# Kernel optimization log

Hardware: AMD Instinct MI355X
Metric: run time of the kernel (lower is better)

The kernel has to match this reference:

```python
import jax, jax.numpy as jnp
import numpy as np

# dims
N, E, H, ED, G = 50000, 1000000, 64, 16, 512
IN_C, OUT_C, L, T, OUT_N = 39, 128, 3, 2, 1
SLOPE = 0.01  # negative slope used by F.leaky_relu and GATConv(negative_slope=0.01)


def _seg_softmax(a, seg, n):
    # numerically-stable softmax over edges grouped by target segment
    m = jax.ops.segment_max(a, seg, num_segments=n)
    m = jnp.where(jnp.isfinite(m), m, 0.0)
    e = jnp.exp(a - m[seg])
    s = jax.ops.segment_sum(e, seg, num_segments=n)
    return e / (s[seg] + 1e-16)


def _gru(inp, h, wi, wh, bi, bh):
    # torch.nn.GRUCell: gates ordered (r, z, n)
    gi = inp @ wi.T + bi
    gh = h @ wh.T + bh
    ir, iz, i_n = jnp.split(gi, 3, axis=-1)
    hr, hz, h_n = jnp.split(gh, 3, axis=-1)
    r = jax.nn.sigmoid(ir + hr)
    z = jax.nn.sigmoid(iz + hz)
    n = jnp.tanh(i_n + r * h_n)
    return (1.0 - z) * n + z * h


def _forward(x, edge_attr,
             lin1_w, lin1_b,
             g_lin1_w, g_att_l, g_att_r, g_lin2_w, g_bias,
             gru0_wi, gru0_wh, gru0_bi, gru0_bh,
             conv_lin_w, conv_att_src, conv_att_dst, conv_bias,
             grul_wi, grul_wh, grul_bi, grul_bh,
             mol_lin_w, mol_att_src, mol_att_dst, mol_bias,
             mgru_wi, mgru_wh, mgru_bi, mgru_bh,
             lin2_w, lin2_b,
             src, dst, batch):
    x = jax.nn.leaky_relu(x @ lin1_w.T + lin1_b, SLOPE)  # [N,H]

    # ---- GATEConv ----
    xj, xi = x[src], x[dst]                               # [E,H]
    t = jax.nn.leaky_relu(jnp.concatenate([xj, edge_attr], -1) @ g_lin1_w.T, SLOPE)
    a = jax.nn.leaky_relu(t @ g_att_l + xi @ g_att_r, SLOPE)
    a = _seg_softmax(a, dst, N)
    h = jax.ops.segment_sum((xj @ g_lin2_w.T) * a[:, None], dst, num_segments=N) + g_bias
    h = jax.nn.elu(h)
    x = jax.nn.relu(_gru(h, x, gru0_wi, gru0_wh, gru0_bi, gru0_bh))

    # ---- GATConv atom layers ----
    for l in range(L - 1):
        hs = x @ conv_lin_w[l].T                          # [N,H]
        a = jax.nn.leaky_relu((hs @ conv_att_src[l])[src] + (hs @ conv_att_dst[l])[dst], SLOPE)
        a = _seg_softmax(a, dst, N)
        h = jax.ops.segment_sum(hs[src] * a[:, None], dst, num_segments=N) + conv_bias[l]
        h = jax.nn.elu(h)
        x = jax.nn.relu(_gru(h, x, grul_wi[l], grul_wh[l], grul_bi[l], grul_bh[l]))

    # ---- molecule-level attention readout ----
    out = jax.nn.relu(jax.ops.segment_sum(x, batch, num_segments=G))  # [G,H]
    for _ in range(T):
        hs = x @ mol_lin_w.T                              # [N,H]  (atoms = sources)
        hd = out @ mol_lin_w.T                            # [G,H]  (mols = targets)
        a = jax.nn.leaky_relu(hs @ mol_att_src + (hd @ mol_att_dst)[batch], SLOPE)
        a = _seg_softmax(a, batch, G)
        h = jax.ops.segment_sum(hs * a[:, None], batch, num_segments=G) + mol_bias
        h = jax.nn.elu(h)
        out = jax.nn.relu(_gru(h, out, mgru_wi, mgru_wh, mgru_bi, mgru_bh))

    out = out @ lin2_w.T + lin2_b                         # [G,OUT_C]
    return jnp.concatenate([out[None]] * OUT_N, axis=0)   # [OUT_N,G,OUT_C]


def setup_inputs() -> dict:
    key = jax.random.key(0)
    it = iter(jax.random.split(key, 48))

    def p(*shape):
        return jax.random.normal(next(it), shape, jnp.float32) * 0.1

    d = {}
    d["x"] = jax.random.normal(next(it), (N, IN_C), jnp.float32)
    d["edge_index"] = jax.random.randint(next(it), (2, E), 0, N, dtype=jnp.int32)
    d["edge_attr"] = jax.random.normal(next(it), (E, ED), jnp.float32)
    d["batch"] = jnp.sort(jax.random.randint(next(it), (N,), 0, G, dtype=jnp.int32))

    d["lin1_w"], d["lin1_b"] = p(H, IN_C), p(H)
    d["g_lin1_w"] = p(H, H + ED)
    d["g_att_l"], d["g_att_r"] = p(H), p(H)
    d["g_lin2_w"], d["g_bias"] = p(H, H), p(H)
    d["gru0_wi"], d["gru0_wh"] = p(3 * H, H), p(3 * H, H)
    d["gru0_bi"], d["gru0_bh"] = p(3 * H), p(3 * H)
    d["conv_lin_w"] = p(L - 1, H, H)
    d["conv_att_src"], d["conv_att_dst"] = p(L - 1, H), p(L - 1, H)
    d["conv_bias"] = p(L - 1, H)
    d["grul_wi"], d["grul_wh"] = p(L - 1, 3 * H, H), p(L - 1, 3 * H, H)
    d["grul_bi"], d["grul_bh"] = p(L - 1, 3 * H), p(L - 1, 3 * H)
    d["mol_lin_w"] = p(H, H)
    d["mol_att_src"], d["mol_att_dst"] = p(H), p(H)
    d["mol_bias"] = p(H)
    d["mgru_wi"], d["mgru_wh"] = p(3 * H, H), p(3 * H, H)
    d["mgru_bi"], d["mgru_bh"] = p(3 * H), p(3 * H)
    d["lin2_w"], d["lin2_b"] = p(OUT_C, H), p(OUT_C)
    return d


def reference(x, edge_index, edge_attr, batch,
              lin1_w, lin1_b,
              g_lin1_w, g_att_l, g_att_r, g_lin2_w, g_bias,
              gru0_wi, gru0_wh, gru0_bi, gru0_bh,
              conv_lin_w, conv_att_src, conv_att_dst, conv_bias,
              grul_wi, grul_wh, grul_bi, grul_bh,
              mol_lin_w, mol_att_src, mol_att_dst, mol_bias,
              mgru_wi, mgru_wh, mgru_bi, mgru_bh,
              lin2_w, lin2_b):
    src, dst = edge_index[0], edge_index[1]
    return _forward(x, edge_attr,
                    lin1_w, lin1_b,
                    g_lin1_w, g_att_l, g_att_r, g_lin2_w, g_bias,
                    gru0_wi, gru0_wh, gru0_bi, gru0_bh,
                    conv_lin_w, conv_att_src, conv_att_dst, conv_bias,
                    grul_wi, grul_wh, grul_bi, grul_bh,
                    mol_lin_w, mol_att_src, mol_att_dst, mol_bias,
                    mgru_wi, mgru_wh, mgru_bi, mgru_bh,
                    lin2_w, lin2_b,
                    src, dst, batch)
```

## Files before the change

### kernel.cpp

```cpp
#include <hip/hip_runtime.h>
#include <math.h>

#define N_NODES 50000
#define N_EDGES 1000000
#define NGRAPH  512
#define INC     39
#define NBKT 196
#define BIN_BLK 4096

typedef __attribute__((ext_vector_type(8))) short bf16x8;
typedef __attribute__((ext_vector_type(4))) float f32x4;
typedef __attribute__((ext_vector_type(4))) int i32x4;

__device__ __forceinline__ float lrelu(float x){ return fmaxf(0.01f*x, x); }
__device__ __forceinline__ float fexp(float x){ return __builtin_amdgcn_exp2f(x*1.4426950408889634f); }
__device__ __forceinline__ float frcp(float x){ return __builtin_amdgcn_rcpf(x); }
__device__ __forceinline__ float eluf (float x){ return x > 0.f ? x : fexp(x) - 1.f; }
__device__ __forceinline__ float sigm (float x){ return frcp(1.f + fexp(-x)); }
__device__ __forceinline__ float ftanh(float x){
  x = fminf(fmaxf(x, -15.f), 15.f);
  float e = __builtin_amdgcn_exp2f(x*2.8853900817779268f);
  return (e - 1.f)*frcp(e + 1.f);
}
__device__ __forceinline__ float rdlane(float v, int l){
  return __int_as_float(__builtin_amdgcn_readlane(__float_as_int(v), l));
}
__device__ __forceinline__ unsigned pk_bf16(float a, float b){
  unsigned r;
  asm volatile("v_cvt_pk_bf16_f32 %0, %1, %2" : "=v"(r) : "v"(a), "v"(b));
  return r;
}
__device__ __forceinline__ float bl(unsigned p){ return __uint_as_float(p << 16); }
__device__ __forceinline__ float bh(unsigned p){ return __uint_as_float(p & 0xffff0000u); }
__device__ __forceinline__ float tobf16f(float v){ return __uint_as_float(pk_bf16(v, 0.f) << 16); }

__global__ __launch_bounds__(256) void k_bhist(const int* __restrict__ dst,
                                               int* __restrict__ bcnt) {
  __shared__ int h[NBKT];
  for (int i = threadIdx.x; i < NBKT; i += 256) h[i] = 0;
  __syncthreads();
  const int e0 = blockIdx.x * BIN_BLK;
  #pragma unroll 4
  for (int u = 0; u < 16; ++u) {
    int e = e0 + u*256 + threadIdx.x;
    if (e < N_EDGES) atomicAdd(&h[dst[e] >> 8], 1);
  }
  __syncthreads();
  for (int i = threadIdx.x; i < NBKT; i += 256) if (h[i]) atomicAdd(&bcnt[i], h[i]);
}

__global__ __launch_bounds__(256) void k_bscan(const int* __restrict__ bcnt,
                                               int* __restrict__ bstart,
                                               int* __restrict__ bcur,
                                               int* __restrict__ rowptrN) {
  __shared__ int s[256];
  int t = threadIdx.x;
  int v = (t < NBKT) ? bcnt[t] : 0;
  s[t] = v; __syncthreads();
  for (int off = 1; off < 256; off <<= 1) {
    int x = (t >= off) ? s[t-off] : 0;
    __syncthreads();
    s[t] += x;
    __syncthreads();
  }
  if (t < NBKT) { int st = s[t] - v; bstart[t] = st; bcur[t] = st; }
  if (t == 0) { bstart[NBKT] = N_EDGES; rowptrN[0] = N_EDGES; }
}

__global__ __launch_bounds__(1024) void k_binA(const int* __restrict__ dst,
                                               const int* __restrict__ src,
                                               const float* __restrict__ p,
                                               int* __restrict__ bcur,
                                               int2* __restrict__ binned) {
  __shared__ int lcnt[NBKT];
  __shared__ int lbase[NBKT];
  __shared__ int gbase[NBKT];
  __shared__ int tmp[256];
  __shared__ int totsh;
  __shared__ int2 stage[BIN_BLK];
  const int t = threadIdx.x;
  const int e0 = blockIdx.x * BIN_BLK;
  for (int i = t; i < NBKT; i += 1024) lcnt[i] = 0;
  __syncthreads();
  int myb[4], myr[4], myd[4], mys[4]; float myp[4];
  #pragma unroll
  for (int u = 0; u < 4; ++u) {
    int e = e0 + u*1024 + t;
    if (e < N_EDGES) {
      int d = dst[e];
      myd[u] = d; mys[u] = src[e]; myp[u] = p[e];
      int b = d >> 8;
      myb[u] = b;
      myr[u] = atomicAdd(&lcnt[b], 1);
    } else myb[u] = -1;
  }
  __syncthreads();
  if (t < 256) tmp[t] = (t < NBKT) ? lcnt[t] : 0;
  __syncthreads();
  for (int off = 1; off < 256; off <<= 1) {
    int v = (t >= off && t < 256) ? tmp[t-off] : 0;
    __syncthreads();
    if (t < 256) tmp[t] += v;
    __syncthreads();
  }
  if (t < NBKT) lbase[t] = tmp[t] - lcnt[t];
  if (t == NBKT-1) totsh = tmp[t];
  if (t < NBKT && lcnt[t] > 0) gbase[t] = atomicAdd(&bcur[t], lcnt[t]);
  __syncthreads();
  #pragma unroll
  for (int u = 0; u < 4; ++u) {
    if (myb[u] >= 0) {
      int x = (mys[u] & 0xffff) | ((myd[u] & 255) << 16) | (myb[u] << 24);
      stage[lbase[myb[u]] + myr[u]] = make_int2(x, __float_as_int(myp[u]));
    }
  }
  __syncthreads();
  const int tot = totsh;
  for (int i = t; i < tot; i += 1024) {
    int2 r = stage[i];
    int b = (unsigned)r.x >> 24;
    binned[gbase[b] + (i - lbase[b])] = r;
  }
}

__global__ __launch_bounds__(1024) void k_binB(const int* __restrict__ bstart,
                                               const int2* __restrict__ binned,
                                               int2* __restrict__ sorted,
                                               int* __restrict__ rowptr) {
  __shared__ int lcnt[256];
  __shared__ int loc[256];
  const int b = blockIdx.x;
  const int base = bstart[b], end = bstart[b+1];
  const int t = threadIdx.x;
  if (t < 256) lcnt[t] = 0;
  __syncthreads();
  for (int i = base + t; i < end; i += 1024)
    atomicAdd(&lcnt[(binned[i].x >> 16) & 255], 1);
  __syncthreads();
  if (t < 256) loc[t] = lcnt[t];
  __syncthreads();
  for (int off = 1; off < 256; off <<= 1) {
    int v = (t >= off && t < 256) ? loc[t-off] : 0;
    __syncthreads();
    if (t < 256) loc[t] += v;
    __syncthreads();
  }
  if (t < 256) {
    int st = base + loc[t] - lcnt[t];
    loc[t] = st;
    int node = b*256 + t;
    if (node < N_NODES) rowptr[node] = st;
    lcnt[t] = 0;
  }
  __syncthreads();
  for (int i = base + t; i < end; i += 1024) {
    int2 r = binned[i];
    int dlow = (r.x >> 16) & 255;
    int rank = atomicAdd(&lcnt[dlow], 1);
    sorted[loc[dlow] + rank] = r;
  }
}

__global__ __launch_bounds__(512) void k_gbound(const int* __restrict__ batch,
                                                int* __restrict__ gstart) {
  int g = threadIdx.x;
  int lo = 0, hi = N_NODES;
  while (lo < hi) { int mid = (lo+hi)>>1; if (batch[mid] < g) lo = mid+1; else hi = mid; }
  gstart[g] = lo;
  if (g == 0) gstart[NGRAPH] = N_NODES;
}

__global__ __launch_bounds__(256) void k_wpack(const float* __restrict__ wi,
                                               const float* __restrict__ wh,
                                               unsigned short* __restrict__ o) {
  int i = blockIdx.x*256 + threadIdx.x;
  if (i < 192*64)      o[i]          = (unsigned short)(pk_bf16(wi[i], 0.f) & 0xffffu);
  else if (i < 2*192*64) o[i]        = (unsigned short)(pk_bf16(wh[i - 192*64], 0.f) & 0xffffu);
}

__global__ __launch_bounds__(256) void k_lin1M(const float* __restrict__ x,
                                               const float* __restrict__ W,
                                               const float* __restrict__ b,
                                               const float* __restrict__ v1,
                                               float* __restrict__ out,
                                               float* __restrict__ o1) {
  const int lane = threadIdx.x & 63;
  const int l15 = lane & 15, lg = lane >> 4;
  const int n0 = blockIdx.x*64 + (threadIdx.x >> 6)*16;
  if (n0 >= N_NODES) return;
  union BF { bf16x8 v; unsigned u[4]; };
  BF Bf[3][4];
  #pragma unroll
  for (int c = 0; c < 3; ++c) {
    int kv0 = c*32 + lg*8;
    int off = (kv0 < 48) ? kv0 : (kv0 - 48);
    int cnt = 39 - off; cnt = cnt < 0 ? 0 : (cnt > 8 ? 8 : cnt);
    #pragma unroll
    for (int ct = 0; ct < 4; ++ct) {
      const float* wrow = W + (ct*16 + l15)*INC;
      float w8[8];
      #pragma unroll
      for (int j = 0; j < 8; ++j) w8[j] = (j < cnt) ? wrow[off+j] : 0.f;
      Bf[c][ct].u[0] = pk_bf16(w8[0], w8[1]);
      Bf[c][ct].u[1] = pk_bf16(w8[2], w8[3]);
      Bf[c][ct].u[2] = pk_bf16(w8[4], w8[5]);
      Bf[c][ct].u[3] = pk_bf16(w8[6], w8[7]);
    }
  }
  const int arow = n0 + l15;
  const bool av = arow < N_NODES;
  const float* xrow = x + (size_t)arow*INC;
  BF A[3];
  #pragma unroll
  for (int c = 0; c < 3; ++c) {
    int kv0 = c*32 + lg*8;
    int islo = (kv0 >= 48);
    int off = islo ? (kv0 - 48) : kv0;
    int cnt = 39 - off; cnt = cnt < 0 ? 0 : (cnt > 8 ? 8 : cnt);
    float a8[8];
    #pragma unroll
    for (int j = 0; j < 8; ++j) {
      float v = (av && j < cnt) ? xrow[off+j] : 0.f;
      if (islo) v = v - tobf16f(v);
      a8[j] = v;
    }
    A[c].u[0] = pk_bf16(a8[0], a8[1]);
    A[c].u[1] = pk_bf16(a8[2], a8[3]);
    A[c].u[2] = pk_bf16(a8[4], a8[5]);
    A[c].u[3] = pk_bf16(a8[6], a8[7]);
  }
  f32x4 acc[4];
  #pragma unroll
  for (int ct = 0; ct < 4; ++ct) acc[ct] = (f32x4){0.f,0.f,0.f,0.f};
  #pragma unroll
  for (int c = 0; c < 3; ++c)
    #pragma unroll
    for (int ct = 0; ct < 4; ++ct)
      acc[ct] = __builtin_amdgcn_mfma_f32_16x16x32_bf16(A[c].v, Bf[c][ct].v, acc[ct], 0, 0, 0);
  float bb[4], attv[4];
  #pragma unroll
  for (int ct = 0; ct < 4; ++ct) { bb[ct] = b[ct*16+l15]; attv[ct] = v1[ct*16+l15]; }
  #pragma unroll
  for (int reg = 0; reg < 4; ++reg) {
    const int node = n0 + 4*lg + reg;
    const bool nv = node < N_NODES;
    float pr = 0.f;
    #pragma unroll
    for (int ct = 0; ct < 4; ++ct) {
      float val = lrelu(acc[ct][reg] + bb[ct]);
      if (nv) out[(size_t)node*64 + ct*16 + l15] = val;
      pr = fmaf(val, attv[ct], pr);
    }
    pr += __shfl_xor(pr, 1, 64);
    pr += __shfl_xor(pr, 2, 64);
    pr += __shfl_xor(pr, 4, 64);
    pr += __shfl_xor(pr, 8, 64);
    if (l15 == 0 && nv) o1[node] = pr;
  }
}

__global__ __launch_bounds__(256) void k_mmdual(const float* __restrict__ in,
                                                const float* __restrict__ W1,
                                                const float* __restrict__ W2,
                                                unsigned short* __restrict__ ubf,
                                                unsigned* __restrict__ ypk, int R) {
  __shared__ float wl[128*65];
  for (int idx = threadIdx.x; idx < 4096; idx += 256) {
    int r = idx >> 6, c = idx & 63;
    wl[r*65+c]      = W1[r*80 + c];
    wl[(64+r)*65+c] = W2[r*64 + c];
  }
  __syncthreads();
  const int lane = threadIdx.x & 63;
  const int base = blockIdx.x*32 + (threadIdx.x>>6)*8;
  float h[8];
  #pragma unroll
  for (int i = 0; i < 8; ++i) { int n = base+i; h[i] = (n < R) ? in[n*64+lane] : 0.f; }
  float accU[8] = {0,0,0,0,0,0,0,0};
  float accY[8] = {0,0,0,0,0,0,0,0};
  for (int k = 0; k < 64; ++k) {
    float wu = wl[lane*65+k], wy = wl[(64+lane)*65+k];
    #pragma unroll
    for (int i = 0; i < 8; ++i) {
      float hk = rdlane(h[i], k);
      accU[i] += hk*wu; accY[i] += hk*wy;
    }
  }
  #pragma unroll
  for (int i = 0; i < 8; ++i) {
    int n = base+i; if (n >= R) continue;
    ubf[n*64 + lane] = (unsigned short)(pk_bf16(accU[i], 0.f) & 0xffffu);
    float partner = __shfl_xor(accY[i], 1, 64);
    if (!(lane & 1)) ypk[n*32 + (lane>>1)] = pk_bf16(accY[i], partner);
  }
}

__global__ __launch_bounds__(256) void k_mm64(const float* __restrict__ in,
                                              const float* __restrict__ W, int rs,
                                              float* __restrict__ out,
                                              unsigned* __restrict__ outp, int R,
                                              const float* __restrict__ v1,
                                              const float* __restrict__ v2,
                                              float* __restrict__ o1,
                                              float* __restrict__ o2) {
  __shared__ float wl[64*65];
  for (int idx = threadIdx.x; idx < 4096; idx += 256) {
    int r = idx >> 6, c = idx & 63;
    wl[r*65+c] = W[r*rs + c];
  }
  __syncthreads();
  const int lane = threadIdx.x & 63;
  const int base = blockIdx.x*32 + (threadIdx.x>>6)*8;
  float h[8];
  #pragma unroll
  for (int i = 0; i < 8; ++i) { int n = base+i; h[i] = (n < R) ? in[n*64+lane] : 0.f; }
  float acc[8] = {0,0,0,0,0,0,0,0};
  for (int k = 0; k < 64; ++k) {
    float wv = wl[lane*65+k];
    #pragma unroll
    for (int i = 0; i < 8; ++i) acc[i] += rdlane(h[i], k) * wv;
  }
  float v1v = v1 ? v1[lane] : 0.f;
  float v2v = v2 ? v2[lane] : 0.f;
  #pragma unroll
  for (int i = 0; i < 8; ++i) {
    int n = base+i; if (n >= R) continue;
    if (out) out[n*64+lane] = acc[i];
    if (outp) {
      float partner = __shfl_xor(acc[i], 1, 64);
      if ((lane & 1) == 0) outp[n*32 + (lane>>1)] = pk_bf16(acc[i], partner);
    }
    if (o1) {
      float p1 = acc[i]*v1v;
      float p2 = acc[i]*v2v;
      #pragma unroll
      for (int s2 = 32; s2 > 0; s2 >>= 1) { p1 += __shfl_xor(p1, s2, 64); p2 += __shfl_xor(p2, s2, 64); }
      if (lane == 0) { o1[n] = p1; if (o2) o2[n] = p2; }
    }
  }
}

__global__ __launch_bounds__(256) void k_escore(const int* __restrict__ srcarr,
                                                const float* __restrict__ ea,
                                                const float* __restrict__ glin1,
                                                const float* __restrict__ attl,
                                                const unsigned short* __restrict__ ubf,
                                                float* __restrict__ pout) {
  const int lane = threadIdx.x & 63;
  const int l15 = lane & 15, lg = lane >> 4;
  const int gw = blockIdx.x*4 + (threadIdx.x >> 6);
  if (gw >= N_EDGES/64) return;
  float attlv[4];
  unsigned Bu[4][2];
  #pragma unroll
  for (int c = 0; c < 4; ++c) {
    const float4 b = *(const float4*)&glin1[(c*16 + l15)*80 + 64 + lg*4];
    Bu[c][0] = pk_bf16(b.x, b.y);
    Bu[c][1] = pk_bf16(b.z, b.w);
    attlv[c] = attl[c*16 + l15];
  }
  const int i0 = gw*64;
  i32x4 sv[4];
  #pragma unroll
  for (int it = 0; it < 4; ++it)
    sv[it] = *(const i32x4*)&srcarr[i0 + it*16 + 4*lg];
  f32x4 a[4];
  #pragma unroll
  for (int it = 0; it < 4; ++it)
    a[it] = __builtin_nontemporal_load((const f32x4*)&ea[(size_t)(i0 + it*16 + l15)*16 + lg*4]);
  unsigned short ug0[4][4], ug1[4][4];
  #pragma unroll
  for (int c = 0; c < 4; ++c)
    #pragma unroll
    for (int r = 0; r < 4; ++r)
      ug0[c][r] = ubf[(size_t)sv[0][r]*64 + c*16 + l15];
  #pragma unroll
  for (int it = 0; it < 4; ++it) {
    if (it + 1 < 4) {
      #pragma unroll
      for (int c = 0; c < 4; ++c)
        #pragma unroll
        for (int r = 0; r < 4; ++r)
          ug1[c][r] = ubf[(size_t)sv[it+1][r]*64 + c*16 + l15];
    }
    union { bf16x8 v; unsigned u[4]; } A;
    A.u[0] = pk_bf16(a[it][0], a[it][1]);
    A.u[1] = pk_bf16(a[it][2], a[it][3]);
    A.u[2] = 0; A.u[3] = 0;
    float p[4] = {0.f,0.f,0.f,0.f};
    #pragma unroll
    for (int c = 0; c < 4; ++c) {
      union { bf16x8 v; unsigned u[4]; } B;
      B.u[0] = Bu[c][0]; B.u[1] = Bu[c][1]; B.u[2] = 0; B.u[3] = 0;
      f32x4 z = {0.f,0.f,0.f,0.f};
      f32x4 acc = __builtin_amdgcn_mfma_f32_16x16x32_bf16(A.v, B.v, z, 0, 0, 0);
      #pragma unroll
      for (int r = 0; r < 4; ++r) {
        float t = lrelu(__uint_as_float(((unsigned)ug0[c][r]) << 16) + acc[r]);
        p[r] = fmaf(t, attlv[c], p[r]);
      }
    }
    #pragma unroll
    for (int r = 0; r < 4; ++r) {
      p[r] += __shfl_xor(p[r], 1, 64);
      p[r] += __shfl_xor(p[r], 2, 64);
      p[r] += __shfl_xor(p[r], 4, 64);
      p[r] += __shfl_xor(p[r], 8, 64);
    }
    if (l15 == 0) {
      f32x4 o = {p[0], p[1], p[2], p[3]};
      __builtin_nontemporal_store(o, (f32x4*)&pout[i0 + it*16 + 4*lg]);
    }
    #pragma unroll
    for (int c = 0; c < 4; ++c)
      #pragma unroll
      for (int r = 0; r < 4; ++r)
        ug0[c][r] = ug1[c][r];
  }
}

__global__ __launch_bounds__(256) void k_gate_agg(const int* __restrict__ rowptr,
                                                  const int2* __restrict__ sorted,
                                                  const float* __restrict__ xr,
                                                  const unsigned* __restrict__ ypk,
                                                  float* __restrict__ hagg) {
  __shared__ int   sS[4][64];
  __shared__ float sE[4][64];
  const int w = __builtin_amdgcn_readfirstlane(threadIdx.x >> 6);
  const int lane = threadIdx.x & 63;
  const int slot = lane >> 5, l2 = lane & 31;
  const int d = blockIdx.x*4 + w;
  const int r0 = __builtin_amdgcn_readfirstlane(rowptr[d]);
  const int r1 = __builtin_amdgcn_readfirstlane(rowptr[d+1]);
  const float xrd = xr[d];
  float accx = 0.f, accy = 0.f, ssum = 0.f;
  for (int base = r0; base < r1; base += 64) {
    int i = base + lane;
    int cnt = r1 - base; if (cnt > 64) cnt = 64;
    float ev = 0.f; int s = 0;
    if (i < r1) {
      int2 r = sorted[i];
      s = r.x & 0xffff;
      ev = fexp(lrelu(__int_as_float(r.y) + xrd));
    }
    sS[w][lane] = s; sE[w][lane] = ev;
    ssum += ev;
    for (int jb = 0; jb < cnt; jb += 16) {
      float e8[8]; unsigned p8[8];
      #pragma unroll
      for (int u = 0; u < 8; ++u) {
        int jj = jb + 2*u + slot;
        int svv; float evv;
        if (jj < cnt) { svv = sS[w][jj]; evv = sE[w][jj]; }
        else          { svv = 0; evv = 0.f; }
        e8[u] = evv;
        p8[u] = ypk[(size_t)svv*32 + l2];
      }
      #pragma unroll
      for (int u = 0; u < 8; ++u) {
        accx = fmaf(e8[u], bl(p8[u]), accx);
        accy = fmaf(e8[u], bh(p8[u]), accy);
      }
    }
  }
  #pragma unroll
  for (int sh = 32; sh > 0; sh >>= 1) ssum += __shfl_xor(ssum, sh, 64);
  accx += __shfl_xor(accx, 32, 64);
  accy += __shfl_xor(accy, 32, 64);
  float rs = frcp(ssum + 1e-16f);
  if (slot == 0) *(float2*)&hagg[d*64 + 2*l2] = make_float2(accx*rs, accy*rs);
}

__global__ __launch_bounds__(256) void k_conv_fused(const int* __restrict__ rowptr,
                                                    const int2* __restrict__ sorted,
                                                    const float* __restrict__ asn,
                                                    const float* __restrict__ adn,
                                                    const unsigned* __restrict__ hsb,
                                                    float* __restrict__ hagg) {
  __shared__ int   sS[4][64];
  __shared__ float sE[4][64];
  const int w = __builtin_amdgcn_readfirstlane(threadIdx.x >> 6);
  const int lane = threadIdx.x & 63;
  const int slot = lane >> 5, l2 = lane & 31;
  const int d = blockIdx.x*4 + w;
  const int r0 = __builtin_amdgcn_readfirstlane(rowptr[d]);
  const int r1 = __builtin_amdgcn_readfirstlane(rowptr[d+1]);
  float adnd = adn[d];
  float accx = 0.f, accy = 0.f, ssum = 0.f;
  for (int base = r0; base < r1; base += 64) {
    int i = base + lane;
    int cnt = r1 - base; if (cnt > 64) cnt = 64;
    float ev = 0.f; int s = 0;
    if (i < r1) { s = sorted[i].x & 0xffff; ev = fexp(lrelu(asn[s] + adnd)); }
    sS[w][lane] = s; sE[w][lane] = ev;
    ssum += ev;
    for (int jb = 0; jb < cnt; jb += 16) {
      float e8[8]; unsigned p8[8];
      #pragma unroll
      for (int u = 0; u < 8; ++u) {
        int jj = jb + 2*u + slot;
        int svv; float evv;
        if (jj < cnt) { svv = sS[w][jj]; evv = sE[w][jj]; }
        else          { svv = 0; evv = 0.f; }
        e8[u] = evv;
        p8[u] = hsb[(size_t)svv*32 + l2];
      }
      #pragma unroll
      for (int u = 0; u < 8; ++u) {
        accx = fmaf(e8[u], bl(p8[u]), accx);
        accy = fmaf(e8[u], bh(p8[u]), accy);
      }
    }
  }
  #pragma unroll
  for (int sh = 32; sh > 0; sh >>= 1) ssum += __shfl_xor(ssum, sh, 64);
  accx += __shfl_xor(accx, 32, 64);
  accy += __shfl_xor(accy, 32, 64);
  float rs = frcp(ssum + 1e-16f);
  if (slot == 0) *(float2*)&hagg[d*64 + 2*l2] = make_float2(accx*rs, accy*rs);
}

__global__ __launch_bounds__(256) void k_gruM(const float* __restrict__ inp,
                                              const float* __restrict__ pbias,
                                              const float* __restrict__ hid,
                                              const unsigned short* __restrict__ wibf,
                                              const unsigned short* __restrict__ whbf,
                                              const float* __restrict__ bi,
                                              const float* __restrict__ bh2,
                                              float* __restrict__ out, int R) {
  const int lane = threadIdx.x & 63;
  const int l15 = lane & 15, lg = lane >> 4;
  const int n0 = blockIdx.x*64 + (threadIdx.x >> 6)*16;
  if (n0 >= R) return;
  union BF { bf16x8 v; unsigned u[4]; };
  BF Ai[2], Ah[2];
  const int arow = n0 + l15;
  const bool av = arow < R;
  const float* ibase = inp + (size_t)arow*64;
  const float* hbase = hid + (size_t)arow*64;
  #pragma unroll
  for (int c = 0; c < 2; ++c) {
    const int k0 = c*32 + lg*8;
    float4 p0 = *(const float4*)&pbias[k0];
    float4 p1 = *(const float4*)&pbias[k0+4];
    float4 v0, v1, h0, h1;
    if (av) {
      v0 = *(const float4*)&ibase[k0];   v1 = *(const float4*)&ibase[k0+4];
      h0 = *(const float4*)&hbase[k0];   h1 = *(const float4*)&hbase[k0+4];
    } else {
      v0 = v1 = h0 = h1 = make_float4(0.f,0.f,0.f,0.f);
      p0 = p1 = make_float4(0.f,0.f,0.f,0.f);
    }
    Ai[c].u[0] = pk_bf16(eluf(v0.x+p0.x), eluf(v0.y+p0.y));
    Ai[c].u[1] = pk_bf16(eluf(v0.z+p0.z), eluf(v0.w+p0.w));
    Ai[c].u[2] = pk_bf16(eluf(v1.x+p1.x), eluf(v1.y+p1.y));
    Ai[c].u[3] = pk_bf16(eluf(v1.z+p1.z), eluf(v1.w+p1.w));
    Ah[c].u[0] = pk_bf16(h0.x, h0.y);
    Ah[c].u[1] = pk_bf16(h0.z, h0.w);
    Ah[c].u[2] = pk_bf16(h1.x, h1.y);
    Ah[c].u[3] = pk_bf16(h1.z, h1.w);
  }
  f32x4 rz[8], ni[4], nh[4];
  #pragma unroll
  for (int t = 0; t < 8; ++t) rz[t] = (f32x4){0.f,0.f,0.f,0.f};
  #pragma unroll
  for (int t = 0; t < 4; ++t) { ni[t] = (f32x4){0.f,0.f,0.f,0.f}; nh[t] = (f32x4){0.f,0.f,0.f,0.f}; }
  #pragma unroll
  for (int t = 0; t < 12; ++t) {
    BF Bi0, Bi1, Bh0, Bh1;
    const size_t off = ((size_t)(t*16 + l15))*64 + lg*8;
    Bi0.v = *(const bf16x8*)&wibf[off];
    Bi1.v = *(const bf16x8*)&wibf[off + 32];
    Bh0.v = *(const bf16x8*)&whbf[off];
    Bh1.v = *(const bf16x8*)&whbf[off + 32];
    if (t < 8) {
      f32x4 a = rz[t];
      a = __builtin_amdgcn_mfma_f32_16x16x32_bf16(Ai[0].v, Bi0.v, a, 0, 0, 0);
      a = __builtin_amdgcn_mfma_f32_16x16x32_bf16(Ai[1].v, Bi1.v, a, 0, 0, 0);
      a = __builtin_amdgcn_mfma_f32_16x16x32_bf16(Ah[0].v, Bh0.v, a, 0, 0, 0);
      a = __builtin_amdgcn_mfma_f32_16x16x32_bf16(Ah[1].v, Bh1.v, a, 0, 0, 0);
      rz[t] = a;
    } else {
      f32x4 a = ni[t-8];
      a = __builtin_amdgcn_mfma_f32_16x16x32_bf16(Ai[0].v, Bi0.v, a, 0, 0, 0);
      a = __builtin_amdgcn_mfma_f32_16x16x32_bf16(Ai[1].v, Bi1.v, a, 0, 0, 0);
      ni[t-8] = a;
      f32x4 b = nh[t-8];
      b = __builtin_amdgcn_mfma_f32_16x16x32_bf16(Ah[0].v, Bh0.v, b, 0, 0, 0);
      b = __builtin_amdgcn_mfma_f32_16x16x32_bf16(Ah[1].v, Bh1.v, b, 0, 0, 0);
      nh[t-8] = b;
    }
  }
  float bsum[8], binv[4], bhnv[4];
  #pragma unroll
  for (int t = 0; t < 8; ++t) bsum[t] = bi[t*16+l15] + bh2[t*16+l15];
  #pragma unroll
  for (int t = 0; t < 4; ++t) {
    binv[t] = bi[128 + t*16 + l15];
    bhnv[t] = bh2[128 + t*16 + l15];
  }
  #pragma unroll
  for (int reg = 0; reg < 4; ++reg) {
    const int node = n0 + 4*lg + reg;
    if (node >= R) continue;
    #pragma unroll
    for (int tt = 0; tt < 4; ++tt) {
      float r  = sigm(rz[tt][reg] + bsum[tt]);
      float z  = sigm(rz[4+tt][reg] + bsum[4+tt]);
      float nn = ftanh(ni[tt][reg] + binv[tt] + r*(nh[tt][reg] + bhnv[tt]));
      float hh = hid[(size_t)node*64 + tt*16 + l15];
      float o  = (1.f - z)*nn + z*hh;
      out[(size_t)node*64 + tt*16 + l15] = fmaxf(o, 0.f);
    }
  }
}

__global__ __launch_bounds__(256) void k_molsum_p(const int* __restrict__ gstart,
                                                  const float* __restrict__ x,
                                                  float* __restrict__ part) {
  int idx = blockIdx.x*4 + (threadIdx.x>>6);
  if (idx >= NGRAPH*8) return;
  int g = idx >> 3, sl = idx & 7;
  int lane = threadIdx.x & 63;
  int n0 = gstart[g], n1 = gstart[g+1];
  int len = n1 - n0;
  int b0 = n0 + (len*sl >> 3), b1 = n0 + (len*(sl+1) >> 3);
  float acc = 0.f;
  for (int n = b0; n < b1; ++n) acc += x[n*64+lane];
  part[idx*64+lane] = acc;
}

__global__ __launch_bounds__(256) void k_molsum_c(const float* __restrict__ part,
                                                  float* __restrict__ outg) {
  int g = blockIdx.x*4 + (threadIdx.x>>6);
  if (g >= NGRAPH) return;
  int lane = threadIdx.x & 63;
  float a = 0.f;
  #pragma unroll
  for (int s = 0; s < 8; ++s) a += part[(g*8+s)*64+lane];
  outg[g*64+lane] = fmaxf(a, 0.f);
}

__global__ __launch_bounds__(256) void k_molhd(const float* __restrict__ outg,
                                               const float* __restrict__ W,
                                               const float* __restrict__ attd,
                                               float* __restrict__ addg) {
  __shared__ float wl[64*65];
  for (int idx = threadIdx.x; idx < 4096; idx += 256) wl[(idx>>6)*65+(idx&63)] = W[idx];
  __syncthreads();
  int g = blockIdx.x*4 + (threadIdx.x>>6);
  if (g >= NGRAPH) return;
  int lane = threadIdx.x & 63;
  float og = outg[g*64+lane];
  float hd = 0.f;
  #pragma unroll
  for (int k = 0; k < 64; ++k) hd += rdlane(og, k) * wl[lane*65+k];
  float p = hd * attd[lane];
  #pragma unroll
  for (int sh = 32; sh > 0; sh >>= 1) p += __shfl_xor(p, sh, 64);
  if (lane == 0) addg[g] = p;
}

__global__ __launch_bounds__(256) void k_molp(const int* __restrict__ gstart,
                                              const float* __restrict__ addg,
                                              const float* __restrict__ asn,
                                              const float* __restrict__ y,
                                              float* __restrict__ part_acc,
                                              float* __restrict__ part_ss) {
  int idx = blockIdx.x*4 + (threadIdx.x>>6);
  if (idx >= NGRAPH*8) return;
  int g = idx >> 3, sl = idx & 7;
  int lane = threadIdx.x & 63;
  int n0 = gstart[g], n1 = gstart[g+1];
  int len = n1 - n0;
  int b0 = n0 + (len*sl >> 3), b1 = n0 + (len*(sl+1) >> 3);
  float adg = addg[g];
  float acc = 0.f, ss = 0.f;
  for (int n = b0; n < b1; ++n) {
    float ev = fexp(lrelu(asn[n] + adg));
    acc += ev * y[n*64+lane];
    ss  += ev;
  }
  part_acc[idx*64+lane] = acc;
  if (lane == 0) part_ss[idx] = ss;
}

__global__ __launch_bounds__(256) void k_molc(const float* __restrict__ part_acc,
                                              const float* __restrict__ part_ss,
                                              float* __restrict__ hg) {
  int g = blockIdx.x*4 + (threadIdx.x>>6);
  if (g >= NGRAPH) return;
  int lane = threadIdx.x & 63;
  float a = 0.f, ss = 0.f;
  #pragma unroll
  for (int s = 0; s < 8; ++s) {
    a  += part_acc[(g*8+s)*64+lane];
    ss += part_ss[g*8+s];
  }
  hg[g*64+lane] = a * frcp(ss + 1e-16f);
}

__global__ __launch_bounds__(128) void k_final(const float* __restrict__ outg,
                                               const float* __restrict__ W,
                                               const float* __restrict__ b,
                                               float* __restrict__ out) {
  __shared__ float og[64];
  int g = blockIdx.x;
  if (threadIdx.x < 64) og[threadIdx.x] = outg[g*64+threadIdx.x];
  __syncthreads();
  int o = threadIdx.x;
  float acc = b[o];
  for (int k = 0; k < 64; ++k) acc += og[k]*W[o*64+k];
  out[g*128+o] = acc;
}

extern "C" void kernel_launch(void* const* d_in, const int* in_sizes, int n_in,
                              void* d_out, int out_size, void* d_ws, size_t ws_size,
                              hipStream_t stream) {
  const float* x_in     = (const float*)d_in[0];
  const int*   eidx     = (const int*)  d_in[1];
  const float* eattr    = (const float*)d_in[2];
  const int*   batch    = (const int*)  d_in[3];
  const float* lin1_w   = (const float*)d_in[4];
  const float* lin1_b   = (const float*)d_in[5];
  const float* g_lin1_w = (const float*)d_in[6];
  const float* g_att_l  = (const float*)d_in[7];
  const float* g_att_r  = (const float*)d_in[8];
  const float* g_lin2_w = (const float*)d_in[9];
  const float* g_bias   = (const float*)d_in[10];
  const float* gru0_wi  = (const float*)d_in[11];
  const float* gru0_wh  = (const float*)d_in[12];
  const float* gru0_bi  = (const float*)d_in[13];
  const float* gru0_bh  = (const float*)d_in[14];
  const float* conv_lin_w   = (const float*)d_in[15];
  const float* conv_att_src = (const float*)d_in[16];
  const float* conv_att_dst = (const float*)d_in[17];
  const float* conv_bias    = (const float*)d_in[18];
  const float* grul_wi  = (const float*)d_in[19];
  const float* grul_wh  = (const float*)d_in[20];
  const float* grul_bi  = (const float*)d_in[21];
  const float* grul_bh  = (const float*)d_in[22];
  const float* mol_lin_w    = (const float*)d_in[23];
  const float* mol_att_src  = (const float*)d_in[24];
  const float* mol_att_dst  = (const float*)d_in[25];
  const float* mol_bias     = (const float*)d_in[26];
  const float* mgru_wi  = (const float*)d_in[27];
  const float* mgru_wh  = (const float*)d_in[28];
  const float* mgru_bi  = (const float*)d_in[29];
  const float* mgru_bh  = (const float*)d_in[30];
  const float* lin2_w   = (const float*)d_in[31];
  const float* lin2_b   = (const float*)d_in[32];

  const int N64 = N_NODES*64;
  float* ws     = (float*)d_ws;
  float* xA     = ws;
  float* xB     = xA + N64;
  float* uy     = xB + N64;
  float* hagg   = uy + 2*N64;
  float* sc1    = hagg + N64;
  float* sc2    = sc1 + N_NODES;
  float* pbuf   = sc2 + N_NODES;
  float* outg   = pbuf + N_EDGES;
  int* bcnt   = (int*)(outg + NGRAPH*64);
  int* rowptr = bcnt + N_NODES;
  int2* binned = (int2*)(rowptr + N_NODES + 2);
  int2* sorted = binned + N_EDGES;
  int* gstart = (int*)(sorted + N_EDGES);
  int* bstart = gstart + NGRAPH+1;
  int* bcur   = bstart + NBKT+1;
  unsigned short* wpk = (unsigned short*)(bcur + NBKT + 4);

  unsigned short* ubf = (unsigned short*)uy;
  unsigned* ypk = (unsigned*)(uy + N64);
  unsigned* hsb = (unsigned*)uy;

  float* part_acc = (float*)binned;
  float* part_ss  = part_acc + NGRAPH*8*64;
  float* addg     = part_ss + NGRAPH*8;

  const int* src = eidx;
  const int* dst = eidx + N_EDGES;

  const int nbN32 = (N_NODES + 31)/32;
  const int nbN4  = (N_NODES + 3)/4;
  const int nbN64 = (N_NODES + 63)/64;
  const int nbG4  = (NGRAPH + 3)/4;
  const int nbG8  = (NGRAPH*8 + 3)/4;
  const int nbES  = (N_EDGES/64 + 3)/4;
  const int nbBIN = (N_EDGES + BIN_BLK-1)/BIN_BLK;
  const int PAIR  = 2*192*64;

  hipMemsetAsync(bcnt, 0, NBKT*sizeof(int), stream);
  k_bhist<<<nbBIN, 256, 0, stream>>>(dst, bcnt);
  k_bscan<<<1, 256, 0, stream>>>(bcnt, bstart, bcur, rowptr + N_NODES);
  k_gbound<<<1, 512, 0, stream>>>(batch, gstart);

  k_wpack<<<(PAIR+255)/256, 256, 0, stream>>>(gru0_wi, gru0_wh, wpk);
  k_wpack<<<(PAIR+255)/256, 256, 0, stream>>>(grul_wi, grul_wh, wpk + PAIR);
  k_wpack<<<(PAIR+255)/256, 256, 0, stream>>>(grul_wi + 192*64, grul_wh + 192*64, wpk + 2*PAIR);
  k_wpack<<<(PAIR+255)/256, 256, 0, stream>>>(mgru_wi, mgru_wh, wpk + 3*PAIR);

  k_lin1M<<<nbN64, 256, 0, stream>>>(x_in, lin1_w, lin1_b, g_att_r, xA, sc1);

  k_mmdual<<<nbN32, 256, 0, stream>>>(xA, g_lin1_w, g_lin2_w, ubf, ypk, N_NODES);
  k_escore<<<nbES, 256, 0, stream>>>(src, eattr, g_lin1_w, g_att_l, ubf, pbuf);
  k_binA<<<nbBIN, 1024, 0, stream>>>(dst, src, pbuf, bcur, binned);
  k_binB<<<NBKT, 1024, 0, stream>>>(bstart, binned, sorted, rowptr);
  k_gate_agg<<<nbN4, 256, 0, stream>>>(rowptr, sorted, sc1, ypk, hagg);
  k_gruM<<<nbN64, 256, 0, stream>>>(hagg, g_bias, xA, wpk, wpk + 192*64,
                                    gru0_bi, gru0_bh, xB, N_NODES);

  float* xcur = xB; float* xoth = xA;

  for (int l = 0; l < 2; ++l) {
    k_mm64<<<nbN32, 256, 0, stream>>>(xcur, conv_lin_w + l*64*64, 64, nullptr, hsb, N_NODES,
                                      conv_att_src + l*64, conv_att_dst + l*64, sc1, sc2);
    k_conv_fused<<<nbN4, 256, 0, stream>>>(rowptr, sorted, sc1, sc2, hsb, hagg);
    k_gruM<<<nbN64, 256, 0, stream>>>(hagg, conv_bias + l*64, xcur,
                                      wpk + (1+l)*PAIR, wpk + (1+l)*PAIR + 192*64,
                                      grul_bi + l*192, grul_bh + l*192, xoth, N_NODES);
    float* t = xcur; xcur = xoth; xoth = t;
  }

  float* ymol = uy;
  k_molsum_p<<<nbG8, 256, 0, stream>>>(gstart, xcur, part_acc);
  k_molsum_c<<<nbG4, 256, 0, stream>>>(part_acc, outg);
  k_mm64<<<nbN32, 256, 0, stream>>>(xcur, mol_lin_w, 64, ymol, nullptr, N_NODES,
                                    mol_att_src, nullptr, sc1, nullptr);
  for (int t = 0; t < 2; ++t) {
    k_molhd<<<nbG4, 256, 0, stream>>>(outg, mol_lin_w, mol_att_dst, addg);
    k_molp<<<nbG8, 256, 0, stream>>>(gstart, addg, sc1, ymol, part_acc, part_ss);
    k_molc<<<nbG4, 256, 0, stream>>>(part_acc, part_ss, hagg);
    k_gruM<<<(NGRAPH+63)/64, 256, 0, stream>>>(hagg, mol_bias, outg,
                                               wpk + 3*PAIR, wpk + 3*PAIR + 192*64,
                                               mgru_bi, mgru_bh, outg, NGRAPH);
  }

  k_final<<<NGRAPH, 128, 0, stream>>>(outg, lin2_w, lin2_b, (float*)d_out);
}
```

Baseline: 454.7 us.

## Use bf16 MFMA for node matmuls and merge small setup kernels

Replaces the scalar readlane-based 64x64 node matmuls (k_mmdual, k_mm64) with MFMA 16x16x32 bf16 versions that load weights straight into registers. For the molecule projection it adds an optional hi/lo split of the input to keep it close to fp32 accuracy. It also merges the bucket scan with the graph-boundary search, and the four weight-pack launches into one, to cut launch overhead. The cost is bf16 rounding of inputs and weights in the conv and gate projections, which lowers precision.

```diff
diff --git a/kernel.cpp b/kernel.cpp
--- a/kernel.cpp
+++ b/kernel.cpp
@@ -7,6 +7,7 @@
 #define INC     39
 #define NBKT 196
 #define BIN_BLK 4096
+#define PAIR_C (2*192*64)
 
 typedef __attribute__((ext_vector_type(8))) short bf16x8;
 typedef __attribute__((ext_vector_type(4))) float f32x4;
@@ -49,22 +50,30 @@
   for (int i = threadIdx.x; i < NBKT; i += 256) if (h[i]) atomicAdd(&bcnt[i], h[i]);
 }
 
-__global__ __launch_bounds__(256) void k_bscan(const int* __restrict__ bcnt,
+__global__ __launch_bounds__(512) void k_setup(const int* __restrict__ bcnt,
                                                int* __restrict__ bstart,
                                                int* __restrict__ bcur,
-                                               int* __restrict__ rowptrN) {
+                                               int* __restrict__ rowptrN,
+                                               const int* __restrict__ batch,
+                                               int* __restrict__ gstart) {
   __shared__ int s[256];
-  int t = threadIdx.x;
-  int v = (t < NBKT) ? bcnt[t] : 0;
-  s[t] = v; __syncthreads();
+  const int t = threadIdx.x;
+  int v = 0;
+  if (t < 256) { v = (t < NBKT) ? bcnt[t] : 0; s[t] = v; }
+  __syncthreads();
   for (int off = 1; off < 256; off <<= 1) {
-    int x = (t >= off) ? s[t-off] : 0;
+    int x = (t >= off && t < 256) ? s[t-off] : 0;
     __syncthreads();
-    s[t] += x;
+    if (t < 256) s[t] += x;
     __syncthreads();
   }
   if (t < NBKT) { int st = s[t] - v; bstart[t] = st; bcur[t] = st; }
   if (t == 0) { bstart[NBKT] = N_EDGES; rowptrN[0] = N_EDGES; }
+  int g = t;
+  int lo = 0, hi = N_NODES;
+  while (lo < hi) { int mid = (lo+hi)>>1; if (batch[mid] < g) lo = mid+1; else hi = mid; }
+  gstart[g] = lo;
+  if (g == 0) gstart[NGRAPH] = N_NODES;
 }
 
 __global__ __launch_bounds__(1024) void k_binA(const int* __restrict__ dst,
@@ -161,21 +170,23 @@
   }
 }
 
-__global__ __launch_bounds__(512) void k_gbound(const int* __restrict__ batch,
-                                                int* __restrict__ gstart) {
-  int g = threadIdx.x;
-  int lo = 0, hi = N_NODES;
-  while (lo < hi) { int mid = (lo+hi)>>1; if (batch[mid] < g) lo = mid+1; else hi = mid; }
-  gstart[g] = lo;
-  if (g == 0) gstart[NGRAPH] = N_NODES;
-}
-
-__global__ __launch_bounds__(256) void k_wpack(const float* __restrict__ wi,
-                                               const float* __restrict__ wh,
-                                               unsigned short* __restrict__ o) {
+__global__ __launch_bounds__(256) void k_wpack4(const float* __restrict__ a0, const float* __restrict__ b0,
+                                                const float* __restrict__ a1, const float* __restrict__ b1,
+                                                const float* __restrict__ a2, const float* __restrict__ b2,
+                                                const float* __restrict__ a3, const float* __restrict__ b3,
+                                                unsigned short* __restrict__ o) {
   int i = blockIdx.x*256 + threadIdx.x;
-  if (i < 192*64)      o[i]          = (unsigned short)(pk_bf16(wi[i], 0.f) & 0xffffu);
-  else if (i < 2*192*64) o[i]        = (unsigned short)(pk_bf16(wh[i - 192*64], 0.f) & 0xffffu);
+  if (i >= 4*PAIR_C) return;
+  int pair = i / PAIR_C;
+  int r = i - pair*PAIR_C;
+  bool hi = r >= 192*64;
+  int rr = hi ? r - 192*64 : r;
+  const float* s;
+  if      (pair == 0) s = hi ? b0 : a0;
+  else if (pair == 1) s = hi ? b1 : a1;
+  else if (pair == 2) s = hi ? b2 : a2;
+  else                s = hi ? b3 : a3;
+  o[i] = (unsigned short)(pk_bf16(s[rr], 0.f) & 0xffffu);
 }
 
 __global__ __launch_bounds__(256) void k_lin1M(const float* __restrict__ x,
@@ -259,83 +270,171 @@
   }
 }
 
-__global__ __launch_bounds__(256) void k_mmdual(const float* __restrict__ in,
-                                                const float* __restrict__ W1,
-                                                const float* __restrict__ W2,
-                                                unsigned short* __restrict__ ubf,
-                                                unsigned* __restrict__ ypk, int R) {
-  __shared__ float wl[128*65];
-  for (int idx = threadIdx.x; idx < 4096; idx += 256) {
-    int r = idx >> 6, c = idx & 63;
-    wl[r*65+c]      = W1[r*80 + c];
-    wl[(64+r)*65+c] = W2[r*64 + c];
-  }
-  __syncthreads();
+__global__ __launch_bounds__(256) void k_mmdualM(const float* __restrict__ in,
+                                                 const float* __restrict__ W1,
+                                                 const float* __restrict__ W2,
+                                                 unsigned* __restrict__ ubf32,
+                                                 unsigned* __restrict__ ypk, int R) {
   const int lane = threadIdx.x & 63;
-  const int base = blockIdx.x*32 + (threadIdx.x>>6)*8;
-  float h[8];
-  #pragma unroll
-  for (int i = 0; i < 8; ++i) { int n = base+i; h[i] = (n < R) ? in[n*64+lane] : 0.f; }
-  float accU[8] = {0,0,0,0,0,0,0,0};
-  float accY[8] = {0,0,0,0,0,0,0,0};
-  for (int k = 0; k < 64; ++k) {
-    float wu = wl[lane*65+k], wy = wl[(64+lane)*65+k];
-    #pragma unroll
-    for (int i = 0; i < 8; ++i) {
-      float hk = rdlane(h[i], k);
-      accU[i] += hk*wu; accY[i] += hk*wy;
-    }
-  }
-  #pragma unroll
-  for (int i = 0; i < 8; ++i) {
-    int n = base+i; if (n >= R) continue;
-    ubf[n*64 + lane] = (unsigned short)(pk_bf16(accU[i], 0.f) & 0xffffu);
-    float partner = __shfl_xor(accY[i], 1, 64);
-    if (!(lane & 1)) ypk[n*32 + (lane>>1)] = pk_bf16(accY[i], partner);
-  }
-}
-
-__global__ __launch_bounds__(256) void k_mm64(const float* __restrict__ in,
-                                              const float* __restrict__ W, int rs,
-                                              float* __restrict__ out,
-                                              unsigned* __restrict__ outp, int R,
-                                              const float* __restrict__ v1,
-                                              const float* __restrict__ v2,
-                                              float* __restrict__ o1,
-                                              float* __restrict__ o2) {
-  __shared__ float wl[64*65];
-  for (int idx = threadIdx.x; idx < 4096; idx += 256) {
-    int r = idx >> 6, c = idx & 63;
-    wl[r*65+c] = W[r*rs + c];
-  }
-  __syncthreads();
+  const int l15 = lane & 15, lg = lane >> 4;
+  const int n0 = blockIdx.x*64 + (threadIdx.x >> 6)*16;
+  if (n0 >= R) return;
+  union BF { bf16x8 v; unsigned u[4]; };
+  BF B1[4][2], B2[4][2];
+  #pragma unroll
+  for (int ct = 0; ct < 4; ++ct) {
+    #pragma unroll
+    for (int c = 0; c < 2; ++c) {
+      const float* w1 = W1 + (size_t)(ct*16 + l15)*80 + c*32 + lg*8;
+      const float* w2 = W2 + (size_t)(ct*16 + l15)*64 + c*32 + lg*8;
+      B1[ct][c].u[0] = pk_bf16(w1[0], w1[1]);
+      B1[ct][c].u[1] = pk_bf16(w1[2], w1[3]);
+      B1[ct][c].u[2] = pk_bf16(w1[4], w1[5]);
+      B1[ct][c].u[3] = pk_bf16(w1[6], w1[7]);
+      B2[ct][c].u[0] = pk_bf16(w2[0], w2[1]);
+      B2[ct][c].u[1] = pk_bf16(w2[2], w2[3]);
+      B2[ct][c].u[2] = pk_bf16(w2[4], w2[5]);
+      B2[ct][c].u[3] = pk_bf16(w2[6], w2[7]);
+    }
+  }
+  const int arow = n0 + l15;
+  const bool av = arow < R;
+  const float* xr = in + (size_t)arow*64;
+  BF A[2];
+  #pragma unroll
+  for (int c = 0; c < 2; ++c) {
+    const int k0 = c*32 + lg*8;
+    float4 v0, v1;
+    if (av) { v0 = *(const float4*)&xr[k0]; v1 = *(const float4*)&xr[k0+4]; }
+    else    { v0 = v1 = make_float4(0.f,0.f,0.f,0.f); }
+    A[c].u[0] = pk_bf16(v0.x, v0.y);
+    A[c].u[1] = pk_bf16(v0.z, v0.w);
+    A[c].u[2] = pk_bf16(v1.x, v1.y);
+    A[c].u[3] = pk_bf16(v1.z, v1.w);
+  }
+  f32x4 aU[4], aY[4];
+  #pragma unroll
+  for (int ct = 0; ct < 4; ++ct) { aU[ct] = (f32x4){0.f,0.f,0.f,0.f}; aY[ct] = (f32x4){0.f,0.f,0.f,0.f}; }
+  #pragma unroll
+  for (int c = 0; c < 2; ++c)
+    #pragma unroll
+    for (int ct = 0; ct < 4; ++ct) {
+      aU[ct] = __builtin_amdgcn_mfma_f32_16x16x32_bf16(A[c].v, B1[ct][c].v, aU[ct], 0, 0, 0);
+      aY[ct] = __builtin_amdgcn_mfma_f32_16x16x32_bf16(A[c].v, B2[ct][c].v, aY[ct], 0, 0, 0);
+    }
+  #pragma unroll
+  for (int reg = 0; reg < 4; ++reg) {
+    const int node = n0 + 4*lg + reg;
+    const bool nv = node < R;
+    #pragma unroll
+    for (int ct = 0; ct < 4; ++ct) {
+      float uu = aU[ct][reg], yy = aY[ct][reg];
+      float up = __shfl_xor(uu, 1, 64);
+      float yp = __shfl_xor(yy, 1, 64);
+      if (!(l15 & 1) && nv) {
+        unsigned idx = (unsigned)node*32 + ct*8 + (l15>>1);
+        ubf32[idx] = pk_bf16(uu, up);
+        ypk[idx]   = pk_bf16(yy, yp);
+      }
+    }
+  }
+}
+
+__global__ __launch_bounds__(256) void k_mm64M(const float* __restrict__ in,
+                                               const float* __restrict__ W, int rs,
+                                               float* __restrict__ out,
+                                               unsigned* __restrict__ outp, int R,
+                                               const float* __restrict__ v1,
+                                               const float* __restrict__ v2,
+                                               float* __restrict__ o1,
+                                               float* __restrict__ o2, int hilo) {
   const int lane = threadIdx.x & 63;
-  const int base = blockIdx.x*32 + (threadIdx.x>>6)*8;
-  float h[8];
-  #pragma unroll
-  for (int i = 0; i < 8; ++i) { int n = base+i; h[i] = (n < R) ? in[n*64+lane] : 0.f; }
-  float acc[8] = {0,0,0,0,0,0,0,0};
-  for (int k = 0; k < 64; ++k) {
-    float wv = wl[lane*65+k];
-    #pragma unroll
-    for (int i = 0; i < 8; ++i) acc[i] += rdlane(h[i], k) * wv;
-  }
-  float v1v = v1 ? v1[lane] : 0.f;
-  float v2v = v2 ? v2[lane] : 0.f;
-  #pragma unroll
-  for (int i = 0; i < 8; ++i) {
-    int n = base+i; if (n >= R) continue;
-    if (out) out[n*64+lane] = acc[i];
-    if (outp) {
-      float partner = __shfl_xor(acc[i], 1, 64);
-      if ((lane & 1) == 0) outp[n*32 + (lane>>1)] = pk_bf16(acc[i], partner);
+  const int l15 = lane & 15, lg = lane >> 4;
+  const int n0 = blockIdx.x*64 + (threadIdx.x >> 6)*16;
+  if (n0 >= R) return;
+  union BF { bf16x8 v; unsigned u[4]; };
+  BF Bf[4][2];
+  #pragma unroll
+  for (int ct = 0; ct < 4; ++ct) {
+    #pragma unroll
+    for (int c = 0; c < 2; ++c) {
+      const float* w = W + (size_t)(ct*16 + l15)*rs + c*32 + lg*8;
+      Bf[ct][c].u[0] = pk_bf16(w[0], w[1]);
+      Bf[ct][c].u[1] = pk_bf16(w[2], w[3]);
+      Bf[ct][c].u[2] = pk_bf16(w[4], w[5]);
+      Bf[ct][c].u[3] = pk_bf16(w[6], w[7]);
+    }
+  }
+  const int arow = n0 + l15;
+  const bool av = arow < R;
+  const float* xr = in + (size_t)arow*64;
+  BF A[2], Alo[2];
+  #pragma unroll
+  for (int c = 0; c < 2; ++c) {
+    const int k0 = c*32 + lg*8;
+    float f[8];
+    if (av) {
+      float4 v0 = *(const float4*)&xr[k0];
+      float4 v1l = *(const float4*)&xr[k0+4];
+      f[0]=v0.x; f[1]=v0.y; f[2]=v0.z; f[3]=v0.w;
+      f[4]=v1l.x; f[5]=v1l.y; f[6]=v1l.z; f[7]=v1l.w;
+    } else {
+      #pragma unroll
+      for (int j = 0; j < 8; ++j) f[j] = 0.f;
+    }
+    A[c].u[0] = pk_bf16(f[0], f[1]);
+    A[c].u[1] = pk_bf16(f[2], f[3]);
+    A[c].u[2] = pk_bf16(f[4], f[5]);
+    A[c].u[3] = pk_bf16(f[6], f[7]);
+    if (hilo) {
+      float l[8];
+      #pragma unroll
+      for (int j = 0; j < 8; ++j) l[j] = f[j] - tobf16f(f[j]);
+      Alo[c].u[0] = pk_bf16(l[0], l[1]);
+      Alo[c].u[1] = pk_bf16(l[2], l[3]);
+      Alo[c].u[2] = pk_bf16(l[4], l[5]);
+      Alo[c].u[3] = pk_bf16(l[6], l[7]);
+    }
+  }
+  f32x4 acc[4];
+  #pragma unroll
+  for (int ct = 0; ct < 4; ++ct) acc[ct] = (f32x4){0.f,0.f,0.f,0.f};
+  #pragma unroll
+  for (int c = 0; c < 2; ++c)
+    #pragma unroll
+    for (int ct = 0; ct < 4; ++ct) {
+      acc[ct] = __builtin_amdgcn_mfma_f32_16x16x32_bf16(A[c].v, Bf[ct][c].v, acc[ct], 0, 0, 0);
+      if (hilo)
+        acc[ct] = __builtin_amdgcn_mfma_f32_16x16x32_bf16(Alo[c].v, Bf[ct][c].v, acc[ct], 0, 0, 0);
+    }
+  float v1v[4], v2v[4];
+  #pragma unroll
+  for (int ct = 0; ct < 4; ++ct) {
+    v1v[ct] = v1 ? v1[ct*16+l15] : 0.f;
+    v2v[ct] = v2 ? v2[ct*16+l15] : 0.f;
+  }
+  #pragma unroll
+  for (int reg = 0; reg < 4; ++reg) {
+    const int node = n0 + 4*lg + reg;
+    const bool nv = node < R;
+    float pr1 = 0.f, pr2 = 0.f;
+    #pragma unroll
+    for (int ct = 0; ct < 4; ++ct) {
+      float val = acc[ct][reg];
+      if (out && nv) out[(size_t)node*64 + ct*16 + l15] = val;
+      if (outp) {
+        float partner = __shfl_xor(val, 1, 64);
+        if (!(l15 & 1) && nv) outp[(unsigned)node*32 + ct*8 + (l15>>1)] = pk_bf16(val, partner);
+      }
+      pr1 = fmaf(val, v1v[ct], pr1);
+      pr2 = fmaf(val, v2v[ct], pr2);
     }
     if (o1) {
-      float p1 = acc[i]*v1v;
-      float p2 = acc[i]*v2v;
-      #pragma unroll
-      for (int s2 = 32; s2 > 0; s2 >>= 1) { p1 += __shfl_xor(p1, s2, 64); p2 += __shfl_xor(p2, s2, 64); }
-      if (lane == 0) { o1[n] = p1; if (o2) o2[n] = p2; }
+      pr1 += __shfl_xor(pr1, 1, 64); pr2 += __shfl_xor(pr2, 1, 64);
+      pr1 += __shfl_xor(pr1, 2, 64); pr2 += __shfl_xor(pr2, 2, 64);
+      pr1 += __shfl_xor(pr1, 4, 64); pr2 += __shfl_xor(pr2, 4, 64);
+      pr1 += __shfl_xor(pr1, 8, 64); pr2 += __shfl_xor(pr2, 8, 64);
+      if (l15 == 0 && nv) { o1[node] = pr1; if (o2) o2[node] = pr2; }
     }
   }
 }
@@ -771,6 +870,7 @@
   unsigned short* wpk = (unsigned short*)(bcur + NBKT + 4);
 
   unsigned short* ubf = (unsigned short*)uy;
+  unsigned* ubf32 = (unsigned*)uy;
   unsigned* ypk = (unsigned*)(uy + N64);
   unsigned* hsb = (unsigned*)uy;
 
@@ -781,28 +881,25 @@
   const int* src = eidx;
   const int* dst = eidx + N_EDGES;
 
-  const int nbN32 = (N_NODES + 31)/32;
   const int nbN4  = (N_NODES + 3)/4;
   const int nbN64 = (N_NODES + 63)/64;
   const int nbG4  = (NGRAPH + 3)/4;
   const int nbG8  = (NGRAPH*8 + 3)/4;
   const int nbES  = (N_EDGES/64 + 3)/4;
   const int nbBIN = (N_EDGES + BIN_BLK-1)/BIN_BLK;
-  const int PAIR  = 2*192*64;
 
   hipMemsetAsync(bcnt, 0, NBKT*sizeof(int), stream);
   k_bhist<<<nbBIN, 256, 0, stream>>>(dst, bcnt);
-  k_bscan<<<1, 256, 0, stream>>>(bcnt, bstart, bcur, rowptr + N_NODES);
-  k_gbound<<<1, 512, 0, stream>>>(batch, gstart);
-
-  k_wpack<<<(PAIR+255)/256, 256, 0, stream>>>(gru0_wi, gru0_wh, wpk);
-  k_wpack<<<(PAIR+255)/256, 256, 0, stream>>>(grul_wi, grul_wh, wpk + PAIR);
-  k_wpack<<<(PAIR+255)/256, 256, 0, stream>>>(grul_wi + 192*64, grul_wh + 192*64, wpk + 2*PAIR);
-  k_wpack<<<(PAIR+255)/256, 256, 0, stream>>>(mgru_wi, mgru_wh, wpk + 3*PAIR);
+  k_setup<<<1, 512, 0, stream>>>(bcnt, bstart, bcur, rowptr + N_NODES, batch, gstart);
+
+  k_wpack4<<<(4*PAIR_C + 255)/256, 256, 0, stream>>>(gru0_wi, gru0_wh,
+                                                     grul_wi, grul_wh,
+                                                     grul_wi + 192*64, grul_wh + 192*64,
+                                                     mgru_wi, mgru_wh, wpk);
 
   k_lin1M<<<nbN64, 256, 0, stream>>>(x_in, lin1_w, lin1_b, g_att_r, xA, sc1);
 
-  k_mmdual<<<nbN32, 256, 0, stream>>>(xA, g_lin1_w, g_lin2_w, ubf, ypk, N_NODES);
+  k_mmdualM<<<nbN64, 256, 0, stream>>>(xA, g_lin1_w, g_lin2_w, ubf32, ypk, N_NODES);
   k_escore<<<nbES, 256, 0, stream>>>(src, eattr, g_lin1_w, g_att_l, ubf, pbuf);
   k_binA<<<nbBIN, 1024, 0, stream>>>(dst, src, pbuf, bcur, binned);
   k_binB<<<NBKT, 1024, 0, stream>>>(bstart, binned, sorted, rowptr);
@@ -813,11 +910,11 @@
   float* xcur = xB; float* xoth = xA;
 
   for (int l = 0; l < 2; ++l) {
-    k_mm64<<<nbN32, 256, 0, stream>>>(xcur, conv_lin_w + l*64*64, 64, nullptr, hsb, N_NODES,
-                                      conv_att_src + l*64, conv_att_dst + l*64, sc1, sc2);
+    k_mm64M<<<nbN64, 256, 0, stream>>>(xcur, conv_lin_w + l*64*64, 64, nullptr, hsb, N_NODES,
+                                       conv_att_src + l*64, conv_att_dst + l*64, sc1, sc2, 0);
     k_conv_fused<<<nbN4, 256, 0, stream>>>(rowptr, sorted, sc1, sc2, hsb, hagg);
     k_gruM<<<nbN64, 256, 0, stream>>>(hagg, conv_bias + l*64, xcur,
-                                      wpk + (1+l)*PAIR, wpk + (1+l)*PAIR + 192*64,
+                                      wpk + (1+l)*PAIR_C, wpk + (1+l)*PAIR_C + 192*64,
                                       grul_bi + l*192, grul_bh + l*192, xoth, N_NODES);
     float* t = xcur; xcur = xoth; xoth = t;
   }
@@ -825,14 +922,14 @@
   float* ymol = uy;
   k_molsum_p<<<nbG8, 256, 0, stream>>>(gstart, xcur, part_acc);
   k_molsum_c<<<nbG4, 256, 0, stream>>>(part_acc, outg);
-  k_mm64<<<nbN32, 256, 0, stream>>>(xcur, mol_lin_w, 64, ymol, nullptr, N_NODES,
-                                    mol_att_src, nullptr, sc1, nullptr);
+  k_mm64M<<<nbN64, 256, 0, stream>>>(xcur, mol_lin_w, 64, ymol, nullptr, N_NODES,
+                                     mol_att_src, nullptr, sc1, nullptr, 1);
   for (int t = 0; t < 2; ++t) {
     k_molhd<<<nbG4, 256, 0, stream>>>(outg, mol_lin_w, mol_att_dst, addg);
     k_molp<<<nbG8, 256, 0, stream>>>(gstart, addg, sc1, ymol, part_acc, part_ss);
     k_molc<<<nbG4, 256, 0, stream>>>(part_acc, part_ss, hagg);
     k_gruM<<<(NGRAPH+63)/64, 256, 0, stream>>>(hagg, mol_bias, outg,
-                                               wpk + 3*PAIR, wpk + 3*PAIR + 192*64,
+                                               wpk + 3*PAIR_C, wpk + 3*PAIR_C + 192*64,
                                                mgru_bi, mgru_bh, outg, NGRAPH);
   }
 
```

After: 419.2 us. 7.8% less time.
